# Optimization experiments

Hardware: AMD Instinct MI355X
Metric: run time of the kernel (lower is better)

## Reference

```python
import jax, jax.numpy as jnp
import numpy as np

B, S, D, H = 16, 256, 1024, 16
HD = D // H          # head_dim = 64
M = 4                # modalities: clip_l, clip_g, t5_xl_l, t5_xl_g
DIMS = [768, 1280, 2048, 2048]
SEQS = [77, 77, 256, 256]

# Hard binding mask: each modality attends to itself and its bound partner.
# Groups: (clip_l <-> t5_xl_l) = indices (0,2); (clip_g <-> t5_xl_g) = (1,3).
_allowed = np.eye(M, dtype=bool)
for _i, _j in [(0, 2), (1, 3)]:
    _allowed[_i, _j] = _allowed[_j, _i] = True
MASK = jnp.asarray(np.where(_allowed, 0.0, -1e9), dtype=jnp.float32)


def setup_inputs() -> dict:
    key = jax.random.key(0)
    ks = iter(jax.random.split(key, 48))
    def n(shape, scale=0.02):
        return jax.random.normal(next(ks), shape, dtype=jnp.float32) * scale
    inp = {}
    names = ["clip_l", "clip_g", "t5_l", "t5_g"]
    for name, d, s in zip(names, DIMS, SEQS):
        inp[f"x_{name}"] = jax.random.normal(next(ks), (B, s, d), dtype=jnp.float32)
        inp[f"Wp_{name}"] = n((d, D))
        inp[f"bp_{name}"] = jnp.zeros((D,), jnp.float32)
    # per-modality alpha gate MLP: Linear(D, D//4) -> GELU -> Linear(D//4, 1) -> Sigmoid
    inp["Wg1"] = n((M, D, D // 4)); inp["bg1"] = jnp.zeros((M, D // 4), jnp.float32)
    inp["Wg2"] = n((M, D // 4, 1)); inp["bg2"] = jnp.zeros((M, 1), jnp.float32)
    inp["alphas"] = jnp.ones((M,), jnp.float32)       # alpha_init = 1.0
    inp["emb"] = n((M, D))                            # modality_embeddings
    inp["Wq"] = n((D, D)); inp["bq"] = jnp.zeros((D,), jnp.float32)
    inp["Wk"] = n((D, D)); inp["bk"] = jnp.zeros((D,), jnp.float32)
    inp["Wv"] = n((D, D)); inp["bv"] = jnp.zeros((D,), jnp.float32)
    inp["temperature"] = jnp.asarray(0.07, jnp.float32)
    inp["betas"] = jnp.full((2,), 0.3, jnp.float32)   # beta_init = 0.3, keys clip_l_t5_xl_l, clip_g_t5_xl_g
    inp["Wout"] = n((M, D, D)); inp["bout"] = jnp.zeros((M, D), jnp.float32)
    return inp


def _forward(x_clip_l, Wp_clip_l, bp_clip_l, x_clip_g, Wp_clip_g, bp_clip_g,
             x_t5_l, Wp_t5_l, bp_t5_l, x_t5_g, Wp_t5_g, bp_t5_g,
             Wg1, bg1, Wg2, bg2, alphas, emb, Wq, bq, Wk, bk, Wv, bv,
             temperature, betas, Wout, bout):
    xs = [x_clip_l, x_clip_g, x_t5_l, x_t5_g]
    Wps = [Wp_clip_l, Wp_clip_g, Wp_t5_l, Wp_t5_g]
    bps = [bp_clip_l, bp_clip_g, bp_t5_l, bp_t5_g]
    projs = []
    for i in range(M):  # fixed small loop over structurally distinct modalities
        p = xs[i] @ Wps[i] + bps[i]                                  # [B, S_i, D]
        h = jax.nn.gelu(p @ Wg1[i] + bg1[i], approximate=False)
        gate = jax.nn.sigmoid(h @ Wg2[i] + bg2[i])                   # [B, S_i, 1]
        a = jax.nn.sigmoid(alphas[i])
        p = p * (gate * a + (1.0 - a)) + emb[i]
        p = jnp.pad(p, ((0, 0), (0, S - p.shape[1]), (0, 0)))        # pad seq to S
        projs.append(p)
    stacked = jnp.stack(projs, axis=1)                               # [B, M, S, D]

    def split(t):  # [B, M, S, D] -> [B, H, M, S, HD]
        return t.reshape(B, M, S, H, HD).transpose(0, 3, 1, 2, 4)
    Q = split(stacked @ Wq + bq)
    K = split(stacked @ Wk + bk)
    V = split(stacked @ Wv + bv)

    # per-position cross-modality attention: scores [B, H, M(target), S, M(source)]
    scores = jnp.einsum('bhmsd,bhwsd->bhmsw', Q, K) / (np.float32(np.sqrt(HD)) * jnp.abs(temperature))
    # beta capacity bias for binding pairs (target -> source): clip_l->t5_xl_l, clip_g->t5_xl_g
    bb = jnp.zeros((M, M), scores.dtype).at[0, 2].set(betas[0]).at[1, 3].set(betas[1])
    scores = scores + (MASK + bb)[None, None, :, None, :]
    attn = jax.nn.softmax(scores, axis=-1)
    ctx = jnp.einsum('bhmsw,bhwsd->bhmsd', attn, V)                  # [B, H, M, S, HD]
    merged = ctx.transpose(0, 2, 3, 1, 4).reshape(B, M, S, D)        # [B, M, S, D]
    out = jnp.einsum('bmsd,mde->bmse', merged, Wout) + bout[:, None, :]
    # per-modality outputs, sliced back to original seq lens, concatenated along seq
    return jnp.concatenate([out[:, i, :SEQS[i]] for i in range(M)], axis=1)  # [B, 666, D]


def reference(x_clip_l, Wp_clip_l, bp_clip_l, x_clip_g, Wp_clip_g, bp_clip_g,
              x_t5_l, Wp_t5_l, bp_t5_l, x_t5_g, Wp_t5_g, bp_t5_g,
              Wg1, bg1, Wg2, bg2, alphas, emb, Wq, bq, Wk, bk, Wv, bv,
              temperature, betas, Wout, bout):
    return _forward(x_clip_l, Wp_clip_l, bp_clip_l, x_clip_g, Wp_clip_g, bp_clip_g,
                    x_t5_l, Wp_t5_l, bp_t5_l, x_t5_g, Wp_t5_g, bp_t5_g,
                    Wg1, bg1, Wg2, bg2, alphas, emb, Wq, bq, Wk, bk, Wv, bv,
                    temperature, betas, Wout, bout)
```

## Files before the change

kernel.cpp:

```cpp
#include <hip/hip_runtime.h>
#include <hip/hip_bf16.h>
#include <math.h>


#define BB 16
#define SS 256
#define DD 1024
#define HH 16
#define HDD 64

typedef __attribute__((ext_vector_type(8))) short bf16x8;
typedef __attribute__((ext_vector_type(4))) float f32x4;
typedef __attribute__((ext_vector_type(4))) unsigned short us4;
typedef __attribute__((ext_vector_type(8))) unsigned short us8;

#define LDA 32

__device__ __forceinline__ int swz(int row, int idx) {
    return idx ^ ((((row) >> 1) & 3) << 3);
}

__device__ __forceinline__ unsigned short f2bf(float x) {
    unsigned u = __float_as_uint(x);
    return (unsigned short)((u + 0x7fffu + ((u >> 16) & 1u)) >> 16);
}
__device__ __forceinline__ float bf2f(unsigned short h) {
    return __uint_as_float((unsigned)h << 16);
}

__global__ __launch_bounds__(256) void wsplit_kernel(
    const float* __restrict__ W, unsigned short* __restrict__ outhi, int K, int N)
{
    __shared__ float t[32][33];
    int kt0 = blockIdx.y << 5, n0 = blockIdx.x << 5;
    int tid = threadIdx.x;
    int r = tid >> 3, c4 = (tid & 7) << 2;
    float4 v = *reinterpret_cast<const float4*>(W + (size_t)(kt0 + r) * N + n0 + c4);
    t[r][c4] = v.x; t[r][c4 + 1] = v.y; t[r][c4 + 2] = v.z; t[r][c4 + 3] = v.w;
    __syncthreads();
    unsigned short* outlo = outhi + (size_t)N * K;
    us4 hv, lv;
#pragma unroll
    for (int j = 0; j < 4; ++j) {
        float x = t[c4 + j][r];
        unsigned short h = f2bf(x);
        hv[j] = h;
        lv[j] = f2bf(x - bf2f(h));
    }
    size_t dst = (size_t)(n0 + r) * K + kt0 + c4;
    *reinterpret_cast<us4*>(outhi + dst) = hv;
    *reinterpret_cast<us4*>(outlo + dst) = lv;
}

__device__ __forceinline__ void mfma_gemm_body(
    const float* __restrict__ A, const unsigned short* __restrict__ Wh,
    const unsigned short* __restrict__ Wl, const float* __restrict__ bias,
    float* __restrict__ C, const int* a_off, const int* c_off,
    int K, int n0, unsigned short* Ah, unsigned short* Al,
    unsigned short* Bh, unsigned short* Bl)
{
    const int tid = threadIdx.x;
    const int lane = tid & 63;
    const int wid = tid >> 6;
    const int wr = wid >> 1, wc = wid & 1;
    const int l15 = lane & 15, l4 = lane >> 4;

    f32x4 acc[4][4];
    const f32x4 zf = {0.0f, 0.0f, 0.0f, 0.0f};
#pragma unroll
    for (int i = 0; i < 4; ++i)
#pragma unroll
        for (int j = 0; j < 4; ++j) acc[i][j] = zf;

    for (int kt = 0; kt < K; kt += 32) {
        __syncthreads();
#pragma unroll
        for (int it = 0; it < 4; ++it) {
            int c = it * 256 + tid;
            int r = c >> 3, k0 = (c & 7) << 2;
            float4 av = *reinterpret_cast<const float4*>(A + a_off[r] + kt + k0);
            float xs[4] = {av.x, av.y, av.z, av.w};
            us4 hv, lv;
#pragma unroll
            for (int q = 0; q < 4; ++q) {
                unsigned short h = f2bf(xs[q]);
                hv[q] = h;
                lv[q] = f2bf(xs[q] - bf2f(h));
            }
            int di = swz(r, r * LDA + k0);
            *reinterpret_cast<us4*>(Ah + di) = hv;
            *reinterpret_cast<us4*>(Al + di) = lv;
        }
#pragma unroll
        for (int it = 0; it < 2; ++it) {
            int c = it * 256 + tid;
            int n = c >> 2, k0 = (c & 3) << 3;
            size_t src = (size_t)(n0 + n) * K + kt + k0;
            int di = swz(n, n * LDA + k0);
            *reinterpret_cast<us8*>(Bh + di) =
                *reinterpret_cast<const us8*>(Wh + src);
            *reinterpret_cast<us8*>(Bl + di) =
                *reinterpret_cast<const us8*>(Wl + src);
        }
        __syncthreads();
        bf16x8 ah[4], al[4];
#pragma unroll
        for (int i = 0; i < 4; ++i) {
            int row = wr * 64 + i * 16 + l15;
            int si = swz(row, row * LDA + l4 * 8);
            ah[i] = *reinterpret_cast<const bf16x8*>(Ah + si);
            al[i] = *reinterpret_cast<const bf16x8*>(Al + si);
        }
#pragma unroll
        for (int j = 0; j < 4; ++j) {
            int ncol = wc * 64 + j * 16 + l15;
            int si = swz(ncol, ncol * LDA + l4 * 8);
            bf16x8 bh = *reinterpret_cast<const bf16x8*>(Bh + si);
            bf16x8 bl = *reinterpret_cast<const bf16x8*>(Bl + si);
#pragma unroll
            for (int i = 0; i < 4; ++i) {
                acc[i][j] = __builtin_amdgcn_mfma_f32_16x16x32_bf16(ah[i], bh, acc[i][j], 0, 0, 0);
                acc[i][j] = __builtin_amdgcn_mfma_f32_16x16x32_bf16(al[i], bh, acc[i][j], 0, 0, 0);
                acc[i][j] = __builtin_amdgcn_mfma_f32_16x16x32_bf16(ah[i], bl, acc[i][j], 0, 0, 0);
            }
        }
    }
#pragma unroll
    for (int j = 0; j < 4; ++j) {
        int col = n0 + wc * 64 + j * 16 + l15;
        float bv = bias[col];
#pragma unroll
        for (int i = 0; i < 4; ++i) {
            int rloc = wr * 64 + i * 16 + l4 * 4;
#pragma unroll
            for (int r = 0; r < 4; ++r) {
                int co = c_off[rloc + r];
                if (co >= 0) C[(size_t)co + col] = acc[i][j][r] + bv;
            }
        }
    }
}

__global__ __launch_bounds__(256) void proj_mfma_kernel(
    const float* __restrict__ x, const unsigned short* __restrict__ Wh,
    const unsigned short* __restrict__ Wl, const float* __restrict__ bp,
    float* __restrict__ stacked, int m, int Sm, int K)
{
    __shared__ unsigned short Ah[128 * LDA], Al[128 * LDA];
    __shared__ unsigned short Bh[128 * LDA], Bl[128 * LDA];
    __shared__ int a_off[128], c_off[128];
    int nrows = BB * Sm;
    int tid = threadIdx.x;
    if (tid < 128) {
        int rg = blockIdx.x * 128 + tid;
        int rc = min(rg, nrows - 1);
        int b = rc / Sm, s = rc - b * Sm;
        a_off[tid] = rc * K;
        c_off[tid] = (rg < nrows) ? (((b * 4 + m) * SS + s) * DD) : -1;
    }
    mfma_gemm_body(x, Wh, Wl, bp, stacked, a_off, c_off, K, blockIdx.y * 128,
                   Ah, Al, Bh, Bl);
}

__global__ __launch_bounds__(256) void lin_mfma_kernel(
    const float* __restrict__ src, const unsigned short* __restrict__ Wh,
    const float* __restrict__ bias, float* __restrict__ C)
{
    __shared__ unsigned short Ah[128 * LDA], Al[128 * LDA];
    __shared__ unsigned short Bh[128 * LDA], Bl[128 * LDA];
    __shared__ int a_off[128], c_off[128];
    int tid = threadIdx.x;
    if (tid < 128) {
        int rg = blockIdx.x * 128 + tid;
        a_off[tid] = rg * DD;
        c_off[tid] = rg * DD;
    }
    mfma_gemm_body(src, Wh, Wh + (size_t)DD * DD, bias, C, a_off, c_off,
                   DD, blockIdx.y * 128, Ah, Al, Bh, Bl);
}

__global__ __launch_bounds__(256) void out_mfma_kernel(
    const float* __restrict__ merged, const unsigned short* __restrict__ Wt_out,
    const float* __restrict__ bout, float* __restrict__ out)
{
    __shared__ unsigned short Ah[128 * LDA], Al[128 * LDA];
    __shared__ unsigned short Bh[128 * LDA], Bl[128 * LDA];
    __shared__ int a_off[128], c_off[128];
    int bx = blockIdx.x;
    int m, t0;
    if (bx < 10)      { m = 0; t0 = bx; }
    else if (bx < 20) { m = 1; t0 = bx - 10; }
    else if (bx < 52) { m = 2; t0 = bx - 20; }
    else              { m = 3; t0 = bx - 52; }
    int Sm  = (m < 2) ? 77 : 256;
    int off = (m == 0) ? 0 : (m == 1) ? 77 : (m == 2) ? 154 : 410;
    int nrows = BB * Sm;
    int tid = threadIdx.x;
    if (tid < 128) {
        int rg = t0 * 128 + tid;
        int rc = min(rg, nrows - 1);
        int b = rc / Sm, s = rc - b * Sm;
        a_off[tid] = ((b * 4 + m) * SS + s) * DD;
        c_off[tid] = (rg < nrows) ? ((b * 666 + off + s) * DD) : -1;
    }
    const unsigned short* Wh = Wt_out + (size_t)m * 2 * DD * DD;
    mfma_gemm_body(merged, Wh, Wh + (size_t)DD * DD, bout + m * DD, out,
                   a_off, c_off, DD, blockIdx.y * 128, Ah, Al, Bh, Bl);
}

__global__ __launch_bounds__(256) void score_kernel(
    const float* __restrict__ Qb, const float* __restrict__ Kb,
    float* __restrict__ Ssc, const float* __restrict__ temp,
    const float* __restrict__ betas)
{
    int bs = blockIdx.x;
    int b = bs >> 8, s = bs & 255;
    int tid = threadIdx.x;
    int m = tid >> 6;
    int h = (tid >> 2) & 15;
    int p = tid & 3;
    int mp = m ^ 2;
    size_t base_s = ((size_t)(b * 4 + m) * SS + s) * DD + h * HDD;
    size_t base_p = ((size_t)(b * 4 + mp) * SS + s) * DD + h * HDD;
    float ss = 0.0f, sc = 0.0f;
#pragma unroll
    for (int i = 0; i < 4; ++i) {
        int d = i * 16 + p * 4;
        float4 q  = *reinterpret_cast<const float4*>(Qb + base_s + d);
        float4 ks = *reinterpret_cast<const float4*>(Kb + base_s + d);
        float4 kc = *reinterpret_cast<const float4*>(Kb + base_p + d);
        ss += q.x * ks.x + q.y * ks.y + q.z * ks.z + q.w * ks.w;
        sc += q.x * kc.x + q.y * kc.y + q.z * kc.z + q.w * kc.w;
    }
    ss += __shfl_xor(ss, 1); ss += __shfl_xor(ss, 2);
    sc += __shfl_xor(sc, 1); sc += __shfl_xor(sc, 2);
    float scale = 1.0f / (8.0f * fabsf(temp[0]));
    ss *= scale;
    sc = sc * scale + ((m == 0) ? betas[0] : (m == 1) ? betas[1] : 0.0f);
    float mx = fmaxf(ss, sc);
    float es = expf(ss - mx), ec = expf(sc - mx);
    float inv = 1.0f / (es + ec);
    if (p == 0) {
        int idx = ((b * 4 + m) * HH + h) * SS + s;
        Ssc[idx] = es * inv;
        Ssc[idx + 262144] = ec * inv;
    }
}

__global__ __launch_bounds__(256) void combine_kernel(
    const float* __restrict__ Ssc, const float* __restrict__ Vb,
    float* __restrict__ merged)
{
    int bs = blockIdx.x;
    int b = bs >> 8, s = bs & 255;
    int tid = threadIdx.x;
    int m = tid >> 6;
    int h = (tid >> 2) & 15;
    int p = tid & 3;
    int mp = m ^ 2;
    size_t base_s = ((size_t)(b * 4 + m) * SS + s) * DD + h * HDD;
    size_t base_p = ((size_t)(b * 4 + mp) * SS + s) * DD + h * HDD;
    int idx = ((b * 4 + m) * HH + h) * SS + s;
    float es = Ssc[idx];
    float ec = Ssc[idx + 262144];
#pragma unroll
    for (int i = 0; i < 4; ++i) {
        int d = i * 16 + p * 4;
        float4 vs = *reinterpret_cast<const float4*>(Vb + base_s + d);
        float4 vc = *reinterpret_cast<const float4*>(Vb + base_p + d);
        float4 o;
        o.x = es * vs.x + ec * vc.x;
        o.y = es * vs.y + ec * vc.y;
        o.z = es * vs.z + ec * vc.z;
        o.w = es * vs.w + ec * vc.w;
        *reinterpret_cast<float4*>(merged + base_s + d) = o;
    }
}

__global__ __launch_bounds__(256) void zero_pad_kernel(float* __restrict__ stacked)
{
    int row = blockIdx.x;
    int m = row / 2864;
    int loc = row - m * 2864;
    int b = loc / 179;
    int s = 77 + (loc - b * 179);
    float4 z; z.x = z.y = z.z = z.w = 0.0f;
    *reinterpret_cast<float4*>(stacked + ((size_t)((b * 4 + m) * SS + s)) * DD +
                               threadIdx.x * 4) = z;
}

__global__ __launch_bounds__(256) void gate_kernel(
    float* __restrict__ P, const float* __restrict__ Wg1,
    const float* __restrict__ bg1, const float* __restrict__ Wg2,
    const float* __restrict__ bg2, const float* __restrict__ alphas,
    const float* __restrict__ emb)
{
    __shared__ float As[16][128];
    __shared__ float wred[4][16];
    __shared__ float scale_s[16];
    __shared__ int rowbase[16];
    int bid = blockIdx.x, tid = threadIdx.x;
    int m, c0;
    if (bid < 77)       { m = 0; c0 = bid; }
    else if (bid < 154) { m = 1; c0 = bid - 77; }
    else if (bid < 410) { m = 2; c0 = bid - 154; }
    else                { m = 3; c0 = bid - 410; }
    int Sm = (m < 2) ? 77 : 256;
    if (tid < 16) {
        int rl = c0 * 16 + tid;
        int b = rl / Sm, s = rl - b * Sm;
        rowbase[tid] = ((b * 4 + m) * SS + s) * DD;
    }
    float acc[16];
#pragma unroll
    for (int r = 0; r < 16; ++r) acc[r] = 0.0f;

    const size_t wbase = (size_t)m * DD * 256;
    for (int kt = 0; kt < DD; kt += 128) {
        __syncthreads();
#pragma unroll
        for (int it = 0; it < 2; ++it) {
            int li = it * 256 + tid;
            int r = li >> 5;
            int q = (li & 31) << 2;
            *reinterpret_cast<float4*>(&As[r][q]) =
                *reinterpret_cast<const float4*>(P + rowbase[r] + kt + q);
        }
        __syncthreads();
        for (int k = 0; k < 128; k += 4) {
            float w0 = Wg1[wbase + (size_t)(kt + k + 0) * 256 + tid];
            float w1 = Wg1[wbase + (size_t)(kt + k + 1) * 256 + tid];
            float w2 = Wg1[wbase + (size_t)(kt + k + 2) * 256 + tid];
            float w3 = Wg1[wbase + (size_t)(kt + k + 3) * 256 + tid];
#pragma unroll
            for (int r = 0; r < 16; ++r) {
                float4 a4 = *reinterpret_cast<const float4*>(&As[r][k]);
                acc[r] = fmaf(a4.x, w0, acc[r]);
                acc[r] = fmaf(a4.y, w1, acc[r]);
                acc[r] = fmaf(a4.z, w2, acc[r]);
                acc[r] = fmaf(a4.w, w3, acc[r]);
            }
        }
    }
    float bg = bg1[m * 256 + tid];
    float w2v = Wg2[m * 256 + tid];
    float part[16];
#pragma unroll
    for (int r = 0; r < 16; ++r) {
        float hv = acc[r] + bg;
        hv = 0.5f * hv * (1.0f + erff(hv * 0.70710678118654752f));
        part[r] = hv * w2v;
    }
#pragma unroll
    for (int r = 0; r < 16; ++r)
        for (int d = 1; d < 64; d <<= 1) part[r] += __shfl_xor(part[r], d);
    int wave = tid >> 6, lane = tid & 63;
    if (lane == 0)
#pragma unroll
        for (int r = 0; r < 16; ++r) wred[wave][r] = part[r];
    __syncthreads();
    if (tid < 16) {
        float g = wred[0][tid] + wred[1][tid] + wred[2][tid] + wred[3][tid] + bg2[m];
        float gate = 1.0f / (1.0f + expf(-g));
        float a = 1.0f / (1.0f + expf(-alphas[m]));
        scale_s[tid] = gate * a + (1.0f - a);
    }
    __syncthreads();
    float4 e4 = *reinterpret_cast<const float4*>(emb + m * DD + tid * 4);
#pragma unroll
    for (int r = 0; r < 16; ++r) {
        float4 v = *reinterpret_cast<float4*>(P + rowbase[r] + tid * 4);
        float sc = scale_s[r];
        v.x = v.x * sc + e4.x; v.y = v.y * sc + e4.y;
        v.z = v.z * sc + e4.z; v.w = v.w * sc + e4.w;
        *reinterpret_cast<float4*>(P + rowbase[r] + tid * 4) = v;
    }
}

#define BM 128
#define BN 128
#define BK 16
#define AST 132

__device__ __forceinline__ void gemm_tile_body(
    const float* __restrict__ A, const float* __restrict__ W,
    const float* __restrict__ bias, float* __restrict__ C,
    const int* a_off, const int* c_off,
    int K, int n0, float* As, float* Bs)
{
    const int tid = threadIdx.x;
    const int tx = tid & 15;
    const int ty = tid >> 4;
    float acc[8][8];
#pragma unroll
    for (int i = 0; i < 8; ++i)
#pragma unroll
        for (int j = 0; j < 8; ++j) acc[i][j] = 0.0f;

    for (int kt = 0; kt < K; kt += BK) {
        __syncthreads();
#pragma unroll
        for (int it = 0; it < 2; ++it) {
            int li = it * 256 + tid;
            int r = li >> 2;
            int kq = (li & 3) << 2;
            float4 av = *reinterpret_cast<const float4*>(A + a_off[r] + kt + kq);
            As[(kq + 0) * AST + r] = av.x;
            As[(kq + 1) * AST + r] = av.y;
            As[(kq + 2) * AST + r] = av.z;
            As[(kq + 3) * AST + r] = av.w;
        }
#pragma unroll
        for (int it = 0; it < 2; ++it) {
            int li = it * 256 + tid;
            int k = li >> 5;
            int nq = (li & 31) << 2;
            *reinterpret_cast<float4*>(Bs + k * BN + nq) =
                *reinterpret_cast<const float4*>(W + (size_t)(kt + k) * DD + n0 + nq);
        }
        __syncthreads();
#pragma unroll
        for (int k = 0; k < BK; ++k) {
            float4 a0 = *reinterpret_cast<const float4*>(As + k * AST + ty * 8);
            float4 a1 = *reinterpret_cast<const float4*>(As + k * AST + ty * 8 + 4);
            float4 b0 = *reinterpret_cast<const float4*>(Bs + k * BN + tx * 8);
            float4 b1 = *reinterpret_cast<const float4*>(Bs + k * BN + tx * 8 + 4);
            float a[8] = {a0.x, a0.y, a0.z, a0.w, a1.x, a1.y, a1.z, a1.w};
            float b[8] = {b0.x, b0.y, b0.z, b0.w, b1.x, b1.y, b1.z, b1.w};
#pragma unroll
            for (int i = 0; i < 8; ++i)
#pragma unroll
                for (int j = 0; j < 8; ++j)
                    acc[i][j] = fmaf(a[i], b[j], acc[i][j]);
        }
    }
    float bv0[8];
#pragma unroll
    for (int j = 0; j < 8; ++j) bv0[j] = bias[n0 + tx * 8 + j];
#pragma unroll
    for (int i = 0; i < 8; ++i) {
        int r = ty * 8 + i;
        int co = c_off[r];
        if (co < 0) continue;
        float* cp = C + (size_t)co + n0 + tx * 8;
        float4 o0, o1;
        o0.x = acc[i][0] + bv0[0]; o0.y = acc[i][1] + bv0[1];
        o0.z = acc[i][2] + bv0[2]; o0.w = acc[i][3] + bv0[3];
        o1.x = acc[i][4] + bv0[4]; o1.y = acc[i][5] + bv0[5];
        o1.z = acc[i][6] + bv0[6]; o1.w = acc[i][7] + bv0[7];
        *reinterpret_cast<float4*>(cp) = o0;
        *reinterpret_cast<float4*>(cp + 4) = o1;
    }
}

__global__ __launch_bounds__(256) void proj_gemm_kernel(
    const float* __restrict__ x, const float* __restrict__ Wp,
    const float* __restrict__ bp, float* __restrict__ stacked,
    int m, int Sm, int K)
{
    __shared__ float As[BK * AST];
    __shared__ float Bs[BK * BN];
    __shared__ int a_off[BM];
    __shared__ int c_off[BM];
    int nrows = BB * Sm;
    int tid = threadIdx.x;
    if (tid < BM) {
        int rg = blockIdx.x * BM + tid;
        int rc = min(rg, nrows - 1);
        int b = rc / Sm, s = rc - b * Sm;
        a_off[tid] = rc * K;
        c_off[tid] = (rg < nrows) ? (((b * 4 + m) * SS + s) * DD) : -1;
    }
    gemm_tile_body(x, Wp, bp, stacked, a_off, c_off, K, blockIdx.y * BN, As, Bs);
}

__global__ __launch_bounds__(256) void qkv_gemm_kernel(
    const float* __restrict__ stacked,
    const float* __restrict__ Wq, const float* __restrict__ bq,
    const float* __restrict__ Wk, const float* __restrict__ bk,
    const float* __restrict__ Wv, const float* __restrict__ bv,
    float* __restrict__ Qo, float* __restrict__ Ko, float* __restrict__ Vo)
{
    __shared__ float As[BK * AST];
    __shared__ float Bs[BK * BN];
    __shared__ int a_off[BM];
    __shared__ int c_off[BM];
    int z = blockIdx.z;
    const float* W = (z == 0) ? Wq : (z == 1) ? Wk : Wv;
    const float* bias = (z == 0) ? bq : (z == 1) ? bk : bv;
    float* C = (z == 0) ? Qo : (z == 1) ? Ko : Vo;
    int tid = threadIdx.x;
    if (tid < BM) {
        int rg = blockIdx.x * BM + tid;
        a_off[tid] = rg * DD;
        c_off[tid] = rg * DD;
    }
    gemm_tile_body(stacked, W, bias, C, a_off, c_off, DD, blockIdx.y * BN, As, Bs);
}

__global__ __launch_bounds__(256) void out_gemm_kernel(
    const float* __restrict__ merged, const float* __restrict__ Wout,
    const float* __restrict__ bout, float* __restrict__ out)
{
    __shared__ float As[BK * AST];
    __shared__ float Bs[BK * BN];
    __shared__ int a_off[BM];
    __shared__ int c_off[BM];
    int bx = blockIdx.x;
    int m, t0;
    if (bx < 10)      { m = 0; t0 = bx; }
    else if (bx < 20) { m = 1; t0 = bx - 10; }
    else if (bx < 52) { m = 2; t0 = bx - 20; }
    else              { m = 3; t0 = bx - 52; }
    int Sm  = (m < 2) ? 77 : 256;
    int off = (m == 0) ? 0 : (m == 1) ? 77 : (m == 2) ? 154 : 410;
    int nrows = BB * Sm;
    int tid = threadIdx.x;
    if (tid < BM) {
        int rg = t0 * BM + tid;
        int rc = min(rg, nrows - 1);
        int b = rc / Sm, s = rc - b * Sm;
        a_off[tid] = ((b * 4 + m) * SS + s) * DD;
        c_off[tid] = (rg < nrows) ? ((b * 666 + off + s) * DD) : -1;
    }
    gemm_tile_body(merged, Wout + (size_t)m * DD * DD, bout + m * DD, out,
                   a_off, c_off, DD, blockIdx.y * BN, As, Bs);
}

__global__ __launch_bounds__(256) void attn_kernel(
    const float* __restrict__ Qb, const float* __restrict__ Kb,
    const float* __restrict__ Vb, float* __restrict__ merged,
    const float* __restrict__ temp, const float* __restrict__ betas)
{
    int bs = blockIdx.x;
    int b = bs >> 8, s = bs & 255;
    int tid = threadIdx.x;
    int m = tid >> 6;
    int h = (tid >> 2) & 15;
    int p = tid & 3;
    int mp = m ^ 2;
    size_t base_s = ((size_t)(b * 4 + m) * SS + s) * DD + h * HDD;
    size_t base_p = ((size_t)(b * 4 + mp) * SS + s) * DD + h * HDD;
    float4 q[4], ks[4], kc[4], vs[4], vc[4];
#pragma unroll
    for (int i = 0; i < 4; ++i) {
        int d = i * 16 + p * 4;
        q[i]  = *reinterpret_cast<const float4*>(Qb + base_s + d);
        ks[i] = *reinterpret_cast<const float4*>(Kb + base_s + d);
        kc[i] = *reinterpret_cast<const float4*>(Kb + base_p + d);
        vs[i] = *reinterpret_cast<const float4*>(Vb + base_s + d);
        vc[i] = *reinterpret_cast<const float4*>(Vb + base_p + d);
    }
    float ss = 0.0f, sc = 0.0f;
#pragma unroll
    for (int i = 0; i < 4; ++i) {
        ss += q[i].x * ks[i].x + q[i].y * ks[i].y + q[i].z * ks[i].z + q[i].w * ks[i].w;
        sc += q[i].x * kc[i].x + q[i].y * kc[i].y + q[i].z * kc[i].z + q[i].w * kc[i].w;
    }
    ss += __shfl_xor(ss, 1); ss += __shfl_xor(ss, 2);
    sc += __shfl_xor(sc, 1); sc += __shfl_xor(sc, 2);
    float scale = 1.0f / (8.0f * fabsf(temp[0]));
    ss *= scale;
    sc = sc * scale + ((m == 0) ? betas[0] : (m == 1) ? betas[1] : 0.0f);
    float mx = fmaxf(ss, sc);
    float es = expf(ss - mx), ec = expf(sc - mx);
    float inv = 1.0f / (es + ec);
    es *= inv; ec *= inv;
#pragma unroll
    for (int i = 0; i < 4; ++i) {
        int d = i * 16 + p * 4;
        float4 o;
        o.x = es * vs[i].x + ec * vc[i].x;
        o.y = es * vs[i].y + ec * vc[i].y;
        o.z = es * vs[i].z + ec * vc[i].z;
        o.w = es * vs[i].w + ec * vc[i].w;
        *reinterpret_cast<float4*>(merged + base_s + d) = o;
    }
}

extern "C" void kernel_launch(void* const* d_in, const int* in_sizes, int n_in,
                              void* d_out, int out_size, void* d_ws, size_t ws_size,
                              hipStream_t stream)
{
    const float* x_cl  = (const float*)d_in[0];
    const float* Wp_cl = (const float*)d_in[1];
    const float* bp_cl = (const float*)d_in[2];
    const float* x_cg  = (const float*)d_in[3];
    const float* Wp_cg = (const float*)d_in[4];
    const float* bp_cg = (const float*)d_in[5];
    const float* x_tl  = (const float*)d_in[6];
    const float* Wp_tl = (const float*)d_in[7];
    const float* bp_tl = (const float*)d_in[8];
    const float* x_tg  = (const float*)d_in[9];
    const float* Wp_tg = (const float*)d_in[10];
    const float* bp_tg = (const float*)d_in[11];
    const float* Wg1   = (const float*)d_in[12];
    const float* bg1   = (const float*)d_in[13];
    const float* Wg2   = (const float*)d_in[14];
    const float* bg2   = (const float*)d_in[15];
    const float* alphas= (const float*)d_in[16];
    const float* emb   = (const float*)d_in[17];
    const float* Wq    = (const float*)d_in[18];
    const float* bq    = (const float*)d_in[19];
    const float* Wk    = (const float*)d_in[20];
    const float* bk    = (const float*)d_in[21];
    const float* Wv    = (const float*)d_in[22];
    const float* bv    = (const float*)d_in[23];
    const float* temp  = (const float*)d_in[24];
    const float* betas = (const float*)d_in[25];
    const float* Wout  = (const float*)d_in[26];
    const float* bout  = (const float*)d_in[27];

    const size_t BUF = (size_t)BB * 4 * SS * DD;
    float* buf0 = (float*)d_ws;
    float* buf1 = buf0 + BUF;
    float* buf2 = buf0 + 2 * BUF;
    float* Ssc  = buf0 + 3 * BUF;

    const size_t OFF_CL  = 0;
    const size_t OFF_CG  = 1572864;
    const size_t OFF_TL  = 4194304;
    const size_t OFF_TG  = 8388608;
    const size_t OFF_Q   = 12582912;
    const size_t OFF_K   = 14680064;
    const size_t OFF_V   = 16777216;
    const size_t OFF_OUT = 18874368;
    const size_t WT_USHORTS = 27262976;
    const size_t NEED = (3 * BUF + 524288) * sizeof(float) + WT_USHORTS * sizeof(unsigned short);

    if (ws_size >= NEED) {
        unsigned short* wt = (unsigned short*)(Ssc + 524288);
        wsplit_kernel<<<dim3(32, 24), 256, 0, stream>>>(Wp_cl, wt + OFF_CL, 768, 1024);
        wsplit_kernel<<<dim3(32, 40), 256, 0, stream>>>(Wp_cg, wt + OFF_CG, 1280, 1024);
        wsplit_kernel<<<dim3(32, 64), 256, 0, stream>>>(Wp_tl, wt + OFF_TL, 2048, 1024);
        wsplit_kernel<<<dim3(32, 64), 256, 0, stream>>>(Wp_tg, wt + OFF_TG, 2048, 1024);
        wsplit_kernel<<<dim3(32, 32), 256, 0, stream>>>(Wq, wt + OFF_Q, 1024, 1024);
        wsplit_kernel<<<dim3(32, 32), 256, 0, stream>>>(Wk, wt + OFF_K, 1024, 1024);
        wsplit_kernel<<<dim3(32, 32), 256, 0, stream>>>(Wv, wt + OFF_V, 1024, 1024);
        for (int m = 0; m < 4; ++m)
            wsplit_kernel<<<dim3(32, 32), 256, 0, stream>>>(
                Wout + (size_t)m * DD * DD, wt + OFF_OUT + (size_t)m * 2 * DD * DD,
                1024, 1024);

        zero_pad_kernel<<<5728, 256, 0, stream>>>(buf0);
        proj_mfma_kernel<<<dim3(10, 8), 256, 0, stream>>>(
            x_cl, wt + OFF_CL, wt + OFF_CL + 786432, bp_cl, buf0, 0, 77, 768);
        proj_mfma_kernel<<<dim3(10, 8), 256, 0, stream>>>(
            x_cg, wt + OFF_CG, wt + OFF_CG + 1310720, bp_cg, buf0, 1, 77, 1280);
        proj_mfma_kernel<<<dim3(32, 8), 256, 0, stream>>>(
            x_tl, wt + OFF_TL, wt + OFF_TL + 2097152, bp_tl, buf0, 2, 256, 2048);
        proj_mfma_kernel<<<dim3(32, 8), 256, 0, stream>>>(
            x_tg, wt + OFF_TG, wt + OFF_TG + 2097152, bp_tg, buf0, 3, 256, 2048);
        gate_kernel<<<666, 256, 0, stream>>>(buf0, Wg1, bg1, Wg2, bg2, alphas, emb);
        lin_mfma_kernel<<<dim3(128, 8), 256, 0, stream>>>(buf0, wt + OFF_Q, bq, buf1);
        lin_mfma_kernel<<<dim3(128, 8), 256, 0, stream>>>(buf0, wt + OFF_K, bk, buf2);
        score_kernel<<<4096, 256, 0, stream>>>(buf1, buf2, Ssc, temp, betas);
        lin_mfma_kernel<<<dim3(128, 8), 256, 0, stream>>>(buf0, wt + OFF_V, bv, buf1);
        combine_kernel<<<4096, 256, 0, stream>>>(Ssc, buf1, buf2);
        out_mfma_kernel<<<dim3(84, 8), 256, 0, stream>>>(buf2, wt + OFF_OUT, bout,
                                                         (float*)d_out);
    } else {
        float* Qb = buf1;
        float* Kb = buf2;
        float* Vb = buf0 + 3 * BUF;
        zero_pad_kernel<<<5728, 256, 0, stream>>>(buf0);
        proj_gemm_kernel<<<dim3(10, 8),  256, 0, stream>>>(x_cl, Wp_cl, bp_cl, buf0, 0, 77, 768);
        proj_gemm_kernel<<<dim3(10, 8),  256, 0, stream>>>(x_cg, Wp_cg, bp_cg, buf0, 1, 77, 1280);
        proj_gemm_kernel<<<dim3(32, 8),  256, 0, stream>>>(x_tl, Wp_tl, bp_tl, buf0, 2, 256, 2048);
        proj_gemm_kernel<<<dim3(32, 8),  256, 0, stream>>>(x_tg, Wp_tg, bp_tg, buf0, 3, 256, 2048);
        gate_kernel<<<666, 256, 0, stream>>>(buf0, Wg1, bg1, Wg2, bg2, alphas, emb);
        qkv_gemm_kernel<<<dim3(128, 8, 3), 256, 0, stream>>>(buf0, Wq, bq, Wk, bk, Wv, bv,
                                                             Qb, Kb, Vb);
        attn_kernel<<<4096, 256, 0, stream>>>(Qb, Kb, Vb, buf0, temp, betas);
        out_gemm_kernel<<<dim3(84, 8), 256, 0, stream>>>(buf0, Wout, bout, (float*)d_out);
    }
}
```

Baseline: 1.270 ms.

## Drop weight low-bf16 term and move gate first layer to MFMA GEMM

Weights are now split only into a high bf16 part, so every MFMA GEMM does two bf16 products per tile instead of three and no longer loads or stages the low weight half. This halves weight memory traffic and LDS use. The gate MLP's first linear layer now runs as a batched MFMA GEMM, followed by a separate kernel that applies GELU, the second projection, the sigmoid scale and the embedding add, replacing the old scalar gate kernel. The cost is lower accuracy from truncating weights to bf16, plus an extra intermediate buffer pass for the gate hidden activations.

```diff
diff --git a/kernel.cpp b/kernel.cpp
--- a/kernel.cpp
+++ b/kernel.cpp
@@ -38,26 +38,17 @@
     float4 v = *reinterpret_cast<const float4*>(W + (size_t)(kt0 + r) * N + n0 + c4);
     t[r][c4] = v.x; t[r][c4 + 1] = v.y; t[r][c4 + 2] = v.z; t[r][c4 + 3] = v.w;
     __syncthreads();
-    unsigned short* outlo = outhi + (size_t)N * K;
-    us4 hv, lv;
-#pragma unroll
-    for (int j = 0; j < 4; ++j) {
-        float x = t[c4 + j][r];
-        unsigned short h = f2bf(x);
-        hv[j] = h;
-        lv[j] = f2bf(x - bf2f(h));
-    }
-    size_t dst = (size_t)(n0 + r) * K + kt0 + c4;
-    *reinterpret_cast<us4*>(outhi + dst) = hv;
-    *reinterpret_cast<us4*>(outlo + dst) = lv;
+    us4 hv;
+#pragma unroll
+    for (int j = 0; j < 4; ++j) hv[j] = f2bf(t[c4 + j][r]);
+    *reinterpret_cast<us4*>(outhi + (size_t)(n0 + r) * K + kt0 + c4) = hv;
 }
 
 __device__ __forceinline__ void mfma_gemm_body(
     const float* __restrict__ A, const unsigned short* __restrict__ Wh,
-    const unsigned short* __restrict__ Wl, const float* __restrict__ bias,
-    float* __restrict__ C, const int* a_off, const int* c_off,
-    int K, int n0, unsigned short* Ah, unsigned short* Al,
-    unsigned short* Bh, unsigned short* Bl)
+    const float* __restrict__ bias, float* __restrict__ C,
+    const int* a_off, const int* c_off,
+    int K, int n0, unsigned short* Ah, unsigned short* Al, unsigned short* Bh)
 {
     const int tid = threadIdx.x;
     const int lane = tid & 63;
@@ -95,12 +86,8 @@
         for (int it = 0; it < 2; ++it) {
             int c = it * 256 + tid;
             int n = c >> 2, k0 = (c & 3) << 3;
-            size_t src = (size_t)(n0 + n) * K + kt + k0;
-            int di = swz(n, n * LDA + k0);
-            *reinterpret_cast<us8*>(Bh + di) =
-                *reinterpret_cast<const us8*>(Wh + src);
-            *reinterpret_cast<us8*>(Bl + di) =
-                *reinterpret_cast<const us8*>(Wl + src);
+            *reinterpret_cast<us8*>(Bh + swz(n, n * LDA + k0)) =
+                *reinterpret_cast<const us8*>(Wh + (size_t)(n0 + n) * K + kt + k0);
         }
         __syncthreads();
         bf16x8 ah[4], al[4];
@@ -114,14 +101,11 @@
 #pragma unroll
         for (int j = 0; j < 4; ++j) {
             int ncol = wc * 64 + j * 16 + l15;
-            int si = swz(ncol, ncol * LDA + l4 * 8);
-            bf16x8 bh = *reinterpret_cast<const bf16x8*>(Bh + si);
-            bf16x8 bl = *reinterpret_cast<const bf16x8*>(Bl + si);
+            bf16x8 bh = *reinterpret_cast<const bf16x8*>(Bh + swz(ncol, ncol * LDA + l4 * 8));
 #pragma unroll
             for (int i = 0; i < 4; ++i) {
                 acc[i][j] = __builtin_amdgcn_mfma_f32_16x16x32_bf16(ah[i], bh, acc[i][j], 0, 0, 0);
                 acc[i][j] = __builtin_amdgcn_mfma_f32_16x16x32_bf16(al[i], bh, acc[i][j], 0, 0, 0);
-                acc[i][j] = __builtin_amdgcn_mfma_f32_16x16x32_bf16(ah[i], bl, acc[i][j], 0, 0, 0);
             }
         }
     }
@@ -143,11 +127,10 @@
 
 __global__ __launch_bounds__(256) void proj_mfma_kernel(
     const float* __restrict__ x, const unsigned short* __restrict__ Wh,
-    const unsigned short* __restrict__ Wl, const float* __restrict__ bp,
-    float* __restrict__ stacked, int m, int Sm, int K)
-{
-    __shared__ unsigned short Ah[128 * LDA], Al[128 * LDA];
-    __shared__ unsigned short Bh[128 * LDA], Bl[128 * LDA];
+    const float* __restrict__ bp, float* __restrict__ stacked,
+    int m, int Sm, int K)
+{
+    __shared__ unsigned short Ah[128 * LDA], Al[128 * LDA], Bh[128 * LDA];
     __shared__ int a_off[128], c_off[128];
     int nrows = BB * Sm;
     int tid = threadIdx.x;
@@ -158,16 +141,15 @@
         a_off[tid] = rc * K;
         c_off[tid] = (rg < nrows) ? (((b * 4 + m) * SS + s) * DD) : -1;
     }
-    mfma_gemm_body(x, Wh, Wl, bp, stacked, a_off, c_off, K, blockIdx.y * 128,
-                   Ah, Al, Bh, Bl);
+    mfma_gemm_body(x, Wh, bp, stacked, a_off, c_off, K, blockIdx.y * 128,
+                   Ah, Al, Bh);
 }
 
 __global__ __launch_bounds__(256) void lin_mfma_kernel(
     const float* __restrict__ src, const unsigned short* __restrict__ Wh,
     const float* __restrict__ bias, float* __restrict__ C)
 {
-    __shared__ unsigned short Ah[128 * LDA], Al[128 * LDA];
-    __shared__ unsigned short Bh[128 * LDA], Bl[128 * LDA];
+    __shared__ unsigned short Ah[128 * LDA], Al[128 * LDA], Bh[128 * LDA];
     __shared__ int a_off[128], c_off[128];
     int tid = threadIdx.x;
     if (tid < 128) {
@@ -175,16 +157,15 @@
         a_off[tid] = rg * DD;
         c_off[tid] = rg * DD;
     }
-    mfma_gemm_body(src, Wh, Wh + (size_t)DD * DD, bias, C, a_off, c_off,
-                   DD, blockIdx.y * 128, Ah, Al, Bh, Bl);
+    mfma_gemm_body(src, Wh, bias, C, a_off, c_off, DD, blockIdx.y * 128,
+                   Ah, Al, Bh);
 }
 
 __global__ __launch_bounds__(256) void out_mfma_kernel(
     const float* __restrict__ merged, const unsigned short* __restrict__ Wt_out,
     const float* __restrict__ bout, float* __restrict__ out)
 {
-    __shared__ unsigned short Ah[128 * LDA], Al[128 * LDA];
-    __shared__ unsigned short Bh[128 * LDA], Bl[128 * LDA];
+    __shared__ unsigned short Ah[128 * LDA], Al[128 * LDA], Bh[128 * LDA];
     __shared__ int a_off[128], c_off[128];
     int bx = blockIdx.x;
     int m, t0;
@@ -203,9 +184,83 @@
         a_off[tid] = ((b * 4 + m) * SS + s) * DD;
         c_off[tid] = (rg < nrows) ? ((b * 666 + off + s) * DD) : -1;
     }
-    const unsigned short* Wh = Wt_out + (size_t)m * 2 * DD * DD;
-    mfma_gemm_body(merged, Wh, Wh + (size_t)DD * DD, bout + m * DD, out,
-                   a_off, c_off, DD, blockIdx.y * 128, Ah, Al, Bh, Bl);
+    mfma_gemm_body(merged, Wt_out + (size_t)m * 1048576, bout + m * DD, out,
+                   a_off, c_off, DD, blockIdx.y * 128, Ah, Al, Bh);
+}
+
+__global__ __launch_bounds__(256) void gate1_mfma_kernel(
+    const float* __restrict__ stacked, const unsigned short* __restrict__ WgT,
+    const float* __restrict__ bg1, float* __restrict__ h)
+{
+    __shared__ unsigned short Ah[128 * LDA], Al[128 * LDA], Bh[128 * LDA];
+    __shared__ int a_off[128], c_off[128];
+    int m = (blockIdx.x >> 1) & 3;
+    int tid = threadIdx.x;
+    if (tid < 128) {
+        int rg = blockIdx.x * 128 + tid;
+        a_off[tid] = rg * DD;
+        c_off[tid] = rg * 256;
+    }
+    mfma_gemm_body(stacked, WgT + (size_t)m * 262144, bg1 + m * 256, h,
+                   a_off, c_off, DD, blockIdx.y * 128, Ah, Al, Bh);
+}
+
+__global__ __launch_bounds__(256) void gate2_kernel(
+    float* __restrict__ P, const float* __restrict__ h,
+    const float* __restrict__ Wg2, const float* __restrict__ bg2,
+    const float* __restrict__ alphas, const float* __restrict__ emb)
+{
+    __shared__ float wred[4][16];
+    __shared__ float scale_s[16];
+    __shared__ int rowbase[16];
+    __shared__ int rowh[16];
+    int bid = blockIdx.x, tid = threadIdx.x;
+    int m, c0;
+    if (bid < 77)       { m = 0; c0 = bid; }
+    else if (bid < 154) { m = 1; c0 = bid - 77; }
+    else if (bid < 410) { m = 2; c0 = bid - 154; }
+    else                { m = 3; c0 = bid - 410; }
+    int Sm = (m < 2) ? 77 : 256;
+    if (tid < 16) {
+        int rl = c0 * 16 + tid;
+        int b = rl / Sm, s = rl - b * Sm;
+        int grow = (b * 4 + m) * SS + s;
+        rowbase[tid] = grow * DD;
+        rowh[tid] = grow * 256;
+    }
+    __syncthreads();
+    float w2v = Wg2[m * 256 + tid];
+    float part[16];
+#pragma unroll
+    for (int r = 0; r < 16; ++r) {
+        float hv = h[rowh[r] + tid];
+        hv = 0.5f * hv * (1.0f + erff(hv * 0.70710678118654752f));
+        part[r] = hv * w2v;
+    }
+#pragma unroll
+    for (int r = 0; r < 16; ++r)
+        for (int d = 1; d < 64; d <<= 1) part[r] += __shfl_xor(part[r], d);
+    int wave = tid >> 6, lane = tid & 63;
+    if (lane == 0)
+#pragma unroll
+        for (int r = 0; r < 16; ++r) wred[wave][r] = part[r];
+    __syncthreads();
+    if (tid < 16) {
+        float g = wred[0][tid] + wred[1][tid] + wred[2][tid] + wred[3][tid] + bg2[m];
+        float gate = 1.0f / (1.0f + expf(-g));
+        float a = 1.0f / (1.0f + expf(-alphas[m]));
+        scale_s[tid] = gate * a + (1.0f - a);
+    }
+    __syncthreads();
+    float4 e4 = *reinterpret_cast<const float4*>(emb + m * DD + tid * 4);
+#pragma unroll
+    for (int r = 0; r < 16; ++r) {
+        float4 v = *reinterpret_cast<float4*>(P + rowbase[r] + tid * 4);
+        float sc = scale_s[r];
+        v.x = v.x * sc + e4.x; v.y = v.y * sc + e4.y;
+        v.z = v.z * sc + e4.z; v.w = v.w * sc + e4.w;
+        *reinterpret_cast<float4*>(P + rowbase[r] + tid * 4) = v;
+    }
 }
 
 __global__ __launch_bounds__(256) void score_kernel(
@@ -287,6 +342,156 @@
     float4 z; z.x = z.y = z.z = z.w = 0.0f;
     *reinterpret_cast<float4*>(stacked + ((size_t)((b * 4 + m) * SS + s)) * DD +
                                threadIdx.x * 4) = z;
+}
+
+#define BM 128
+#define BN 128
+#define BK 16
+#define AST 132
+
+__device__ __forceinline__ void gemm_tile_body(
+    const float* __restrict__ A, const float* __restrict__ W,
+    const float* __restrict__ bias, float* __restrict__ C,
+    const int* a_off, const int* c_off,
+    int K, int n0, float* As, float* Bs)
+{
+    const int tid = threadIdx.x;
+    const int tx = tid & 15;
+    const int ty = tid >> 4;
+    float acc[8][8];
+#pragma unroll
+    for (int i = 0; i < 8; ++i)
+#pragma unroll
+        for (int j = 0; j < 8; ++j) acc[i][j] = 0.0f;
+
+    for (int kt = 0; kt < K; kt += BK) {
+        __syncthreads();
+#pragma unroll
+        for (int it = 0; it < 2; ++it) {
+            int li = it * 256 + tid;
+            int r = li >> 2;
+            int kq = (li & 3) << 2;
+            float4 av = *reinterpret_cast<const float4*>(A + a_off[r] + kt + kq);
+            As[(kq + 0) * AST + r] = av.x;
+            As[(kq + 1) * AST + r] = av.y;
+            As[(kq + 2) * AST + r] = av.z;
+            As[(kq + 3) * AST + r] = av.w;
+        }
+#pragma unroll
+        for (int it = 0; it < 2; ++it) {
+            int li = it * 256 + tid;
+            int k = li >> 5;
+            int nq = (li & 31) << 2;
+            *reinterpret_cast<float4*>(Bs + k * BN + nq) =
+                *reinterpret_cast<const float4*>(W + (size_t)(kt + k) * DD + n0 + nq);
+        }
+        __syncthreads();
+#pragma unroll
+        for (int k = 0; k < BK; ++k) {
+            float4 a0 = *reinterpret_cast<const float4*>(As + k * AST + ty * 8);
+            float4 a1 = *reinterpret_cast<const float4*>(As + k * AST + ty * 8 + 4);
+            float4 b0 = *reinterpret_cast<const float4*>(Bs + k * BN + tx * 8);
+            float4 b1 = *reinterpret_cast<const float4*>(Bs + k * BN + tx * 8 + 4);
+            float a[8] = {a0.x, a0.y, a0.z, a0.w, a1.x, a1.y, a1.z, a1.w};
+            float b[8] = {b0.x, b0.y, b0.z, b0.w, b1.x, b1.y, b1.z, b1.w};
+#pragma unroll
+            for (int i = 0; i < 8; ++i)
+#pragma unroll
+                for (int j = 0; j < 8; ++j)
+                    acc[i][j] = fmaf(a[i], b[j], acc[i][j]);
+        }
+    }
+    float bv0[8];
+#pragma unroll
+    for (int j = 0; j < 8; ++j) bv0[j] = bias[n0 + tx * 8 + j];
+#pragma unroll
+    for (int i = 0; i < 8; ++i) {
+        int r = ty * 8 + i;
+        int co = c_off[r];
+        if (co < 0) continue;
+        float* cp = C + (size_t)co + n0 + tx * 8;
+        float4 o0, o1;
+        o0.x = acc[i][0] + bv0[0]; o0.y = acc[i][1] + bv0[1];
+        o0.z = acc[i][2] + bv0[2]; o0.w = acc[i][3] + bv0[3];
+        o1.x = acc[i][4] + bv0[4]; o1.y = acc[i][5] + bv0[5];
+        o1.z = acc[i][6] + bv0[6]; o1.w = acc[i][7] + bv0[7];
+        *reinterpret_cast<float4*>(cp) = o0;
+        *reinterpret_cast<float4*>(cp + 4) = o1;
+    }
+}
+
+__global__ __launch_bounds__(256) void proj_gemm_kernel(
+    const float* __restrict__ x, const float* __restrict__ Wp,
+    const float* __restrict__ bp, float* __restrict__ stacked,
+    int m, int Sm, int K)
+{
+    __shared__ float As[BK * AST];
+    __shared__ float Bs[BK * BN];
+    __shared__ int a_off[BM];
+    __shared__ int c_off[BM];
+    int nrows = BB * Sm;
+    int tid = threadIdx.x;
+    if (tid < BM) {
+        int rg = blockIdx.x * BM + tid;
+        int rc = min(rg, nrows - 1);
+        int b = rc / Sm, s = rc - b * Sm;
+        a_off[tid] = rc * K;
+        c_off[tid] = (rg < nrows) ? (((b * 4 + m) * SS + s) * DD) : -1;
+    }
+    gemm_tile_body(x, Wp, bp, stacked, a_off, c_off, K, blockIdx.y * BN, As, Bs);
+}
+
+__global__ __launch_bounds__(256) void qkv_gemm_kernel(
+    const float* __restrict__ stacked,
+    const float* __restrict__ Wq, const float* __restrict__ bq,
+    const float* __restrict__ Wk, const float* __restrict__ bk,
+    const float* __restrict__ Wv, const float* __restrict__ bv,
+    float* __restrict__ Qo, float* __restrict__ Ko, float* __restrict__ Vo)
+{
+    __shared__ float As[BK * AST];
+    __shared__ float Bs[BK * BN];
+    __shared__ int a_off[BM];
+    __shared__ int c_off[BM];
+    int z = blockIdx.z;
+    const float* W = (z == 0) ? Wq : (z == 1) ? Wk : Wv;
+    const float* bias = (z == 0) ? bq : (z == 1) ? bk : bv;
+    float* C = (z == 0) ? Qo : (z == 1) ? Ko : Vo;
+    int tid = threadIdx.x;
+    if (tid < BM) {
+        int rg = blockIdx.x * BM + tid;
+        a_off[tid] = rg * DD;
+        c_off[tid] = rg * DD;
+    }
+    gemm_tile_body(stacked, W, bias, C, a_off, c_off, DD, blockIdx.y * BN, As, Bs);
+}
+
+__global__ __launch_bounds__(256) void out_gemm_kernel(
+    const float* __restrict__ merged, const float* __restrict__ Wout,
+    const float* __restrict__ bout, float* __restrict__ out)
+{
+    __shared__ float As[BK * AST];
+    __shared__ float Bs[BK * BN];
+    __shared__ int a_off[BM];
+    __shared__ int c_off[BM];
+    int bx = blockIdx.x;
+    int m, t0;
+    if (bx < 10)      { m = 0; t0 = bx; }
+    else if (bx < 20) { m = 1; t0 = bx - 10; }
+    else if (bx < 52) { m = 2; t0 = bx - 20; }
+    else              { m = 3; t0 = bx - 52; }
+    int Sm  = (m < 2) ? 77 : 256;
+    int off = (m == 0) ? 0 : (m == 1) ? 77 : (m == 2) ? 154 : 410;
+    int nrows = BB * Sm;
+    int tid = threadIdx.x;
+    if (tid < BM) {
+        int rg = t0 * BM + tid;
+        int rc = min(rg, nrows - 1);
+        int b = rc / Sm, s = rc - b * Sm;
+        a_off[tid] = ((b * 4 + m) * SS + s) * DD;
+        c_off[tid] = (rg < nrows) ? ((b * 666 + off + s) * DD) : -1;
+    }
+    gemm_tile_body(merged, Wout + (size_t)m * DD * DD, bout + m * DD, out,
+                   a_off, c_off, DD, blockIdx.y * BN, As, Bs);
 }
 
 __global__ __launch_bounds__(256) void gate_kernel(
@@ -375,156 +580,6 @@
         v.z = v.z * sc + e4.z; v.w = v.w * sc + e4.w;
         *reinterpret_cast<float4*>(P + rowbase[r] + tid * 4) = v;
     }
-}
-
-#define BM 128
-#define BN 128
-#define BK 16
-#define AST 132
-
-__device__ __forceinline__ void gemm_tile_body(
-    const float* __restrict__ A, const float* __restrict__ W,
-    const float* __restrict__ bias, float* __restrict__ C,
-    const int* a_off, const int* c_off,
-    int K, int n0, float* As, float* Bs)
-{
-    const int tid = threadIdx.x;
-    const int tx = tid & 15;
-    const int ty = tid >> 4;
-    float acc[8][8];
-#pragma unroll
-    for (int i = 0; i < 8; ++i)
-#pragma unroll
-        for (int j = 0; j < 8; ++j) acc[i][j] = 0.0f;
-
-    for (int kt = 0; kt < K; kt += BK) {
-        __syncthreads();
-#pragma unroll
-        for (int it = 0; it < 2; ++it) {
-            int li = it * 256 + tid;
-            int r = li >> 2;
-            int kq = (li & 3) << 2;
-            float4 av = *reinterpret_cast<const float4*>(A + a_off[r] + kt + kq);
-            As[(kq + 0) * AST + r] = av.x;
-            As[(kq + 1) * AST + r] = av.y;
-            As[(kq + 2) * AST + r] = av.z;
-            As[(kq + 3) * AST + r] = av.w;
-        }
-#pragma unroll
-        for (int it = 0; it < 2; ++it) {
-            int li = it * 256 + tid;
-            int k = li >> 5;
-            int nq = (li & 31) << 2;
-            *reinterpret_cast<float4*>(Bs + k * BN + nq) =
-                *reinterpret_cast<const float4*>(W + (size_t)(kt + k) * DD + n0 + nq);
-        }
-        __syncthreads();
-#pragma unroll
-        for (int k = 0; k < BK; ++k) {
-            float4 a0 = *reinterpret_cast<const float4*>(As + k * AST + ty * 8);
-            float4 a1 = *reinterpret_cast<const float4*>(As + k * AST + ty * 8 + 4);
-            float4 b0 = *reinterpret_cast<const float4*>(Bs + k * BN + tx * 8);
-            float4 b1 = *reinterpret_cast<const float4*>(Bs + k * BN + tx * 8 + 4);
-            float a[8] = {a0.x, a0.y, a0.z, a0.w, a1.x, a1.y, a1.z, a1.w};
-            float b[8] = {b0.x, b0.y, b0.z, b0.w, b1.x, b1.y, b1.z, b1.w};
-#pragma unroll
-            for (int i = 0; i < 8; ++i)
-#pragma unroll
-                for (int j = 0; j < 8; ++j)
-                    acc[i][j] = fmaf(a[i], b[j], acc[i][j]);
-        }
-    }
-    float bv0[8];
-#pragma unroll
-    for (int j = 0; j < 8; ++j) bv0[j] = bias[n0 + tx * 8 + j];
-#pragma unroll
-    for (int i = 0; i < 8; ++i) {
-        int r = ty * 8 + i;
-        int co = c_off[r];
-        if (co < 0) continue;
-        float* cp = C + (size_t)co + n0 + tx * 8;
-        float4 o0, o1;
-        o0.x = acc[i][0] + bv0[0]; o0.y = acc[i][1] + bv0[1];
-        o0.z = acc[i][2] + bv0[2]; o0.w = acc[i][3] + bv0[3];
-        o1.x = acc[i][4] + bv0[4]; o1.y = acc[i][5] + bv0[5];
-        o1.z = acc[i][6] + bv0[6]; o1.w = acc[i][7] + bv0[7];
-        *reinterpret_cast<float4*>(cp) = o0;
-        *reinterpret_cast<float4*>(cp + 4) = o1;
-    }
-}
-
-__global__ __launch_bounds__(256) void proj_gemm_kernel(
-    const float* __restrict__ x, const float* __restrict__ Wp,
-    const float* __restrict__ bp, float* __restrict__ stacked,
-    int m, int Sm, int K)
-{
-    __shared__ float As[BK * AST];
-    __shared__ float Bs[BK * BN];
-    __shared__ int a_off[BM];
-    __shared__ int c_off[BM];
-    int nrows = BB * Sm;
-    int tid = threadIdx.x;
-    if (tid < BM) {
-        int rg = blockIdx.x * BM + tid;
-        int rc = min(rg, nrows - 1);
-        int b = rc / Sm, s = rc - b * Sm;
-        a_off[tid] = rc * K;
-        c_off[tid] = (rg < nrows) ? (((b * 4 + m) * SS + s) * DD) : -1;
-    }
-    gemm_tile_body(x, Wp, bp, stacked, a_off, c_off, K, blockIdx.y * BN, As, Bs);
-}
-
-__global__ __launch_bounds__(256) void qkv_gemm_kernel(
-    const float* __restrict__ stacked,
-    const float* __restrict__ Wq, const float* __restrict__ bq,
-    const float* __restrict__ Wk, const float* __restrict__ bk,
-    const float* __restrict__ Wv, const float* __restrict__ bv,
-    float* __restrict__ Qo, float* __restrict__ Ko, float* __restrict__ Vo)
-{
-    __shared__ float As[BK * AST];
-    __shared__ float Bs[BK * BN];
-    __shared__ int a_off[BM];
-    __shared__ int c_off[BM];
-    int z = blockIdx.z;
-    const float* W = (z == 0) ? Wq : (z == 1) ? Wk : Wv;
-    const float* bias = (z == 0) ? bq : (z == 1) ? bk : bv;
-    float* C = (z == 0) ? Qo : (z == 1) ? Ko : Vo;
-    int tid = threadIdx.x;
-    if (tid < BM) {
-        int rg = blockIdx.x * BM + tid;
-        a_off[tid] = rg * DD;
-        c_off[tid] = rg * DD;
-    }
-    gemm_tile_body(stacked, W, bias, C, a_off, c_off, DD, blockIdx.y * BN, As, Bs);
-}
-
-__global__ __launch_bounds__(256) void out_gemm_kernel(
-    const float* __restrict__ merged, const float* __restrict__ Wout,
-    const float* __restrict__ bout, float* __restrict__ out)
-{
-    __shared__ float As[BK * AST];
-    __shared__ float Bs[BK * BN];
-    __shared__ int a_off[BM];
-    __shared__ int c_off[BM];
-    int bx = blockIdx.x;
-    int m, t0;
-    if (bx < 10)      { m = 0; t0 = bx; }
-    else if (bx < 20) { m = 1; t0 = bx - 10; }
-    else if (bx < 52) { m = 2; t0 = bx - 20; }
-    else              { m = 3; t0 = bx - 52; }
-    int Sm  = (m < 2) ? 77 : 256;
-    int off = (m == 0) ? 0 : (m == 1) ? 77 : (m == 2) ? 154 : 410;
-    int nrows = BB * Sm;
-    int tid = threadIdx.x;
-    if (tid < BM) {
-        int rg = t0 * BM + tid;
-        int rc = min(rg, nrows - 1);
-        int b = rc / Sm, s = rc - b * Sm;
-        a_off[tid] = ((b * 4 + m) * SS + s) * DD;
-        c_off[tid] = (rg < nrows) ? ((b * 666 + off + s) * DD) : -1;
-    }
-    gemm_tile_body(merged, Wout + (size_t)m * DD * DD, bout + m * DD, out,
-                   a_off, c_off, DD, blockIdx.y * BN, As, Bs);
 }
 
 __global__ __launch_bounds__(256) void attn_kernel(
@@ -618,14 +673,15 @@
     float* Ssc  = buf0 + 3 * BUF;
 
     const size_t OFF_CL  = 0;
-    const size_t OFF_CG  = 1572864;
-    const size_t OFF_TL  = 4194304;
-    const size_t OFF_TG  = 8388608;
-    const size_t OFF_Q   = 12582912;
-    const size_t OFF_K   = 14680064;
-    const size_t OFF_V   = 16777216;
-    const size_t OFF_OUT = 18874368;
-    const size_t WT_USHORTS = 27262976;
+    const size_t OFF_CG  = 786432;
+    const size_t OFF_TL  = 2097152;
+    const size_t OFF_TG  = 4194304;
+    const size_t OFF_Q   = 6291456;
+    const size_t OFF_K   = 7340032;
+    const size_t OFF_V   = 8388608;
+    const size_t OFF_OUT = 9437184;
+    const size_t OFF_WG1 = 13631488;
+    const size_t WT_USHORTS = 14680064;
     const size_t NEED = (3 * BUF + 524288) * sizeof(float) + WT_USHORTS * sizeof(unsigned short);
 
     if (ws_size >= NEED) {
@@ -639,19 +695,25 @@
         wsplit_kernel<<<dim3(32, 32), 256, 0, stream>>>(Wv, wt + OFF_V, 1024, 1024);
         for (int m = 0; m < 4; ++m)
             wsplit_kernel<<<dim3(32, 32), 256, 0, stream>>>(
-                Wout + (size_t)m * DD * DD, wt + OFF_OUT + (size_t)m * 2 * DD * DD,
+                Wout + (size_t)m * DD * DD, wt + OFF_OUT + (size_t)m * 1048576,
                 1024, 1024);
+        for (int m = 0; m < 4; ++m)
+            wsplit_kernel<<<dim3(8, 32), 256, 0, stream>>>(
+                Wg1 + (size_t)m * DD * 256, wt + OFF_WG1 + (size_t)m * 262144,
+                1024, 256);
 
         zero_pad_kernel<<<5728, 256, 0, stream>>>(buf0);
         proj_mfma_kernel<<<dim3(10, 8), 256, 0, stream>>>(
-            x_cl, wt + OFF_CL, wt + OFF_CL + 786432, bp_cl, buf0, 0, 77, 768);
+            x_cl, wt + OFF_CL, bp_cl, buf0, 0, 77, 768);
         proj_mfma_kernel<<<dim3(10, 8), 256, 0, stream>>>(
-            x_cg, wt + OFF_CG, wt + OFF_CG + 1310720, bp_cg, buf0, 1, 77, 1280);
+            x_cg, wt + OFF_CG, bp_cg, buf0, 1, 77, 1280);
         proj_mfma_kernel<<<dim3(32, 8), 256, 0, stream>>>(
-            x_tl, wt + OFF_TL, wt + OFF_TL + 2097152, bp_tl, buf0, 2, 256, 2048);
+            x_tl, wt + OFF_TL, bp_tl, buf0, 2, 256, 2048);
         proj_mfma_kernel<<<dim3(32, 8), 256, 0, stream>>>(
-            x_tg, wt + OFF_TG, wt + OFF_TG + 2097152, bp_tg, buf0, 3, 256, 2048);
-        gate_kernel<<<666, 256, 0, stream>>>(buf0, Wg1, bg1, Wg2, bg2, alphas, emb);
+            x_tg, wt + OFF_TG, bp_tg, buf0, 3, 256, 2048);
+        gate1_mfma_kernel<<<dim3(128, 2), 256, 0, stream>>>(buf0, wt + OFF_WG1,
+                                                            bg1, buf1);
+        gate2_kernel<<<666, 256, 0, stream>>>(buf0, buf1, Wg2, bg2, alphas, emb);
         lin_mfma_kernel<<<dim3(128, 8), 256, 0, stream>>>(buf0, wt + OFF_Q, bq, buf1);
         lin_mfma_kernel<<<dim3(128, 8), 256, 0, stream>>>(buf0, wt + OFF_K, bk, buf2);
         score_kernel<<<4096, 256, 0, stream>>>(buf1, buf2, Ssc, temp, betas);
```

Result: faster. 1.056 ms (-16.9%).
